# Performance work log

Hardware: AMD Instinct MI355X
Metric: run time of the kernel (lower is better)

Reference implementation:

```python
import jax, jax.numpy as jnp
import numpy as np

THRESH = 0.3   # vis_threshold (score filter and final keep threshold)
SIGMA = 0.5    # Gaussian soft-NMS sigma (method=2 in classic soft_nms)
B, N = 16, 2048


def setup_inputs() -> dict:
    key = jax.random.key(0)
    k1, k2, k3 = jax.random.split(key, 3)
    xy = jax.random.uniform(k1, (B, N, 2), dtype=jnp.float32) * 1024.0
    wh = jax.random.uniform(k2, (B, N, 2), dtype=jnp.float32) * 256.0 + 1.0
    scores = jax.random.uniform(k3, (B, N, 1), dtype=jnp.float32)
    detections = jnp.concatenate([xy, xy + wh, scores], axis=-1)  # [B,N,5]
    return {"detections": detections}


def _pairwise_iou(b):
    # b: [N,4] as (x1,y1,x2,y2); classic soft-NMS uses +1 area convention
    x1, y1, x2, y2 = b[:, 0], b[:, 1], b[:, 2], b[:, 3]
    area = (x2 - x1 + 1.0) * (y2 - y1 + 1.0)
    xx1 = jnp.maximum(x1[:, None], x1[None, :])
    yy1 = jnp.maximum(y1[:, None], y1[None, :])
    xx2 = jnp.minimum(x2[:, None], x2[None, :])
    yy2 = jnp.minimum(y2[:, None], y2[None, :])
    w = jnp.clip(xx2 - xx1 + 1.0, 0.0)
    h = jnp.clip(yy2 - yy1 + 1.0, 0.0)
    inter = w * h
    return inter / (area[:, None] + area[None, :] - inter)  # [N,N]


def _soft_nms_single(boxes, scores):
    # boxes: [N,4], scores: [N]
    n = scores.shape[0]
    iou = _pairwise_iou(boxes)            # [N,N]
    valid = scores > THRESH               # score-threshold prefilter
    s0 = jnp.where(valid, scores, 0.0)

    def step(carry, _):
        s, active = carry
        i = jnp.argmax(jnp.where(active, s, -1.0))     # greedy pick of max live score
        si = jnp.where(active[i], s[i], -1.0)          # -1 sentinel once all boxes consumed
        w = jnp.exp(-(iou[i] * iou[i]) / SIGMA)        # Gaussian decay (method=2)
        active = active.at[i].set(False)
        s = jnp.where(active, s * w, s)                # decay remaining live scores
        return (s, active), (i, si)

    _, (idx, picked) = jax.lax.scan(step, (s0, valid), None, length=n)
    # score each box carried at the moment it was picked; .max ignores -1 sentinels
    final = jnp.full((n,), -1.0, scores.dtype).at[idx].max(picked)
    keep = final > THRESH
    return final, keep


def reference(detections):
    boxes = detections[..., :4]   # [B,N,4]
    scores = detections[..., 4]   # [B,N]
    final, keep = jax.vmap(_soft_nms_single)(boxes, scores)
    return final, keep
```

## Files before the change

### kernel.cpp

```cpp
#include <hip/hip_runtime.h>
#include <stdint.h>

static constexpr float kThresh = 0.3f;
static constexpr float kFreeze = 0.0195f;
static constexpr int N    = 2048;
static constexpr int NT   = 256;
static constexpr int LPT  = N / NT;
static constexpr int NW   = NT / 64;
static constexpr int KMAX = 8;

using u64 = unsigned long long;
using u32 = unsigned int;

template <int CTRL>
__device__ __forceinline__ u64 dpp_max_u64_step(u64 k) {
    const int lo  = (int)(u32)k;
    const int hi  = (int)(u32)(k >> 32);
    const int mlo = __builtin_amdgcn_update_dpp(lo, lo, CTRL, 0xF, 0xF, false);
    const int mhi = __builtin_amdgcn_update_dpp(hi, hi, CTRL, 0xF, 0xF, false);
    const u64 m   = ((u64)(u32)mhi << 32) | (u32)mlo;
    return (m > k) ? m : k;
}
__device__ __forceinline__ u64 wave_max_u64(u64 k) {
    k = dpp_max_u64_step<0x111>(k);
    k = dpp_max_u64_step<0x112>(k);
    k = dpp_max_u64_step<0x114>(k);
    k = dpp_max_u64_step<0x118>(k);
    k = dpp_max_u64_step<0x142>(k);
    k = dpp_max_u64_step<0x143>(k);
    const int lo = __builtin_amdgcn_readlane((int)(u32)k, 63);
    const int hi = __builtin_amdgcn_readlane((int)(u32)(k >> 32), 63);
    return ((u64)(u32)hi << 32) | (u32)lo;
}

struct Pick {
    u32    mid;
    float4 box;
    float  area;
};

template <int K>
__device__ __forceinline__ u64 decay_and_keys(
        float (&sr)[KMAX], const float (&x1)[KMAX], const float (&y1)[KMAX],
        const float (&x2)[KMAX], const float (&y2)[KMAX], const float (&ar)[KMAX],
        const u32 (&jp)[KMAX], const Pick& w)
{
    u64 kmax = 0ULL;
    #pragma unroll
    for (int e = 0; e < K; ++e) {
        if (jp[e] == w.mid) sr[e] = -1.0f;
        const float xx1 = fmaxf(w.box.x, x1[e]);
        const float yy1 = fmaxf(w.box.y, y1[e]);
        const float xx2 = fminf(w.box.z, x2[e]);
        const float yy2 = fminf(w.box.w, y2[e]);
        const float ww  = fmaxf(xx2 - xx1 + 1.0f, 0.0f);
        const float hh  = fmaxf(yy2 - yy1 + 1.0f, 0.0f);
        const float inter = ww * hh;
        const float iou   = inter / (w.area + ar[e] - inter);
        sr[e] *= expf(-(iou * iou) * 2.0f);
        const u64 key = ((u64)(__float_as_uint(sr[e]) + 1u) << 32) | jp[e];
        const u64 kk  = (__float_as_int(sr[e]) >= 0) ? key : 0ULL;
        if (kk > kmax) kmax = kk;
    }
    return kmax;
}

template <int K>
__device__ __forceinline__ void fill_slots(
        float (&sr)[KMAX], float (&x1)[KMAX], float (&y1)[KMAX],
        float (&x2)[KMAX], float (&y2)[KMAX], float (&ar)[KMAX], u32 (&jp)[KMAX],
        const int* slist, const float* srs, const float4* sbox, int t, int alive)
{
    #pragma unroll
    for (int e = 0; e < K; ++e) {
        const int pos = t + NT * e;
        if (pos < alive) {
            const int j = slist[pos];
            sr[e] = srs[pos];
            const float4 bb = sbox[j];
            x1[e] = bb.x; y1[e] = bb.y; x2[e] = bb.z; y2[e] = bb.w;
            ar[e] = (bb.z - bb.x + 1.0f) * (bb.w - bb.y + 1.0f);
            jp[e] = ((u32)(N - 1 - j) << 21) | ((u32)t << 13) | ((u32)e << 10);
        } else {
            sr[e] = -1.0f;
            x1[e] = 3.0e38f; y1[e] = 3.0e38f; x2[e] = -3.0e38f; y2[e] = -3.0e38f;
            ar[e] = 1.0f;
            jp[e] = 0x3FFu;
        }
    }
}

template <int K>
__device__ __forceinline__ void run_tier(
        int& alive, int& k, Pick& w,
        float (&sr)[KMAX], float (&x1)[KMAX], float (&y1)[KMAX],
        float (&x2)[KMAX], float (&y2)[KMAX], float (&ar)[KMAX], u32 (&jp)[KMAX],
        int* slist, float* srs, const float4* sbox, float* sfin,
        u64 (*redk)[NW], int* swave, int t, int lane, int wid)
{
    const int floorA = (K > 1) ? NT * (K - 1) : 0;
    if (alive <= floorA) return;

    fill_slots<K>(sr, x1, y1, x2, y2, ar, jp, slist, srs, sbox, t, alive);
    const int tierFill = alive;

    while (alive > floorA) {
        const int par = k & 1;
        const u64 kmax = decay_and_keys<K>(sr, x1, y1, x2, y2, ar, jp, w);
        const u64 wmax = wave_max_u64(kmax);
        const bool writer = (wmax != 0ULL) ? (kmax == wmax) : (lane == 0);
        if (writer) redk[par][wid] = wmax;
        __syncthreads();
        u64 best = redk[par][0];
        #pragma unroll
        for (int q = 1; q < NW; ++q) {
            const u64 o = redk[par][q];
            if (o > best) best = o;
        }
        const u32   lo = (u32)best;
        const float v1 = __uint_as_float((u32)(best >> 32) - 1u);

        if (v1 < kFreeze) {
            #pragma unroll
            for (int e = 0; e < K; ++e) {
                const int pos = t + NT * e;
                if (pos < tierFill && __float_as_int(sr[e]) >= 0)
                    sfin[(N - 1) - (int)(jp[e] >> 21)] = sr[e];
            }
            alive = -1;
            return;
        }

        const int winJ = (N - 1) - (int)(lo >> 21);
        w.mid = lo;
        if (t == 0) sfin[winJ] = v1;
        w.box  = sbox[winJ];
        w.area = (w.box.z - w.box.x + 1.0f) * (w.box.w - w.box.y + 1.0f);
        --alive; ++k;
    }

    if (K > 1) {
        (void)decay_and_keys<K>(sr, x1, y1, x2, y2, ar, jp, w);
        w.mid  = 0xFFFFFFFFu;
        w.box  = make_float4(3.0e38f, 3.0e38f, -3.0e38f, -3.0e38f);
        w.area = 1.0f;
        int c = 0;
        #pragma unroll
        for (int e = 0; e < K; ++e) c += (__float_as_int(sr[e]) >= 0) ? 1 : 0;
        int pfx = c;
        #pragma unroll
        for (int d = 1; d < 64; d <<= 1) {
            const int v = __shfl_up(pfx, d, 64);
            if (lane >= d) pfx += v;
        }
        if (lane == 63) swave[wid] = pfx;
        __syncthreads();
        int wbase = 0;
        #pragma unroll
        for (int q = 0; q < NW; ++q)
            if (q < wid) wbase += swave[q];
        int mypos = wbase + (pfx - c);
        #pragma unroll
        for (int e = 0; e < K; ++e) {
            if (__float_as_int(sr[e]) >= 0) {
                slist[mypos] = (N - 1) - (int)(jp[e] >> 21);
                srs[mypos]   = sr[e];
                ++mypos;
            }
        }
        __syncthreads();
    }
}

__launch_bounds__(NT, 1)
__global__ void soft_nms_kernel(const float* __restrict__ det,
                                float* __restrict__ out, int B)
{
    const int b = blockIdx.x, t = threadIdx.x, lane = t & 63, wid = t >> 6;

    __shared__ float4 sbox[N];
    __shared__ float  sfin[N];
    __shared__ float  srs[N];
    __shared__ int    slist[N];
    __shared__ int    swave[NW];
    __shared__ u64    redk[2][NW];

    const float* dbase = det + (size_t)b * N * 5;

    float scv[LPT]; int lval = 0, c = 0;
    #pragma unroll
    for (int e = 0; e < LPT; ++e) {
        const int j = t * LPT + e;
        const float* p = dbase + (size_t)j * 5;
        const float X1 = p[0], Y1 = p[1], X2 = p[2], Y2 = p[3], SC = p[4];
        sbox[j]  = make_float4(X1, Y1, X2, Y2);
        sfin[j]  = -1.0f;
        scv[e]   = SC;
        const int va = SC > kThresh;
        lval |= va << e; c += va;
    }
    int pfx = c;
    #pragma unroll
    for (int d = 1; d < 64; d <<= 1) {
        const int v = __shfl_up(pfx, d, 64);
        if (lane >= d) pfx += v;
    }
    if (lane == 63) swave[wid] = pfx;
    __syncthreads();
    int wbase = 0, n0 = 0;
    #pragma unroll
    for (int q = 0; q < NW; ++q) {
        const int v = swave[q];
        if (q < wid) wbase += v;
        n0 += v;
    }
    int mypos = wbase + (pfx - c);
    #pragma unroll
    for (int e = 0; e < LPT; ++e)
        if ((lval >> e) & 1) { slist[mypos] = t * LPT + e; srs[mypos] = scv[e]; ++mypos; }
    __syncthreads();

    float sr[KMAX], x1[KMAX], y1[KMAX], x2[KMAX], y2[KMAX], ar[KMAX]; u32 jp[KMAX];
    int alive = n0, k = 0;
    Pick w;
    w.mid  = 0xFFFFFFFFu;
    w.box  = make_float4(3.0e38f, 3.0e38f, -3.0e38f, -3.0e38f);
    w.area = 1.0f;

    run_tier<8>(alive,k,w,sr,x1,y1,x2,y2,ar,jp,slist,srs,sbox,sfin,redk,swave,t,lane,wid);
    run_tier<7>(alive,k,w,sr,x1,y1,x2,y2,ar,jp,slist,srs,sbox,sfin,redk,swave,t,lane,wid);
    run_tier<6>(alive,k,w,sr,x1,y1,x2,y2,ar,jp,slist,srs,sbox,sfin,redk,swave,t,lane,wid);
    run_tier<5>(alive,k,w,sr,x1,y1,x2,y2,ar,jp,slist,srs,sbox,sfin,redk,swave,t,lane,wid);
    run_tier<4>(alive,k,w,sr,x1,y1,x2,y2,ar,jp,slist,srs,sbox,sfin,redk,swave,t,lane,wid);
    run_tier<3>(alive,k,w,sr,x1,y1,x2,y2,ar,jp,slist,srs,sbox,sfin,redk,swave,t,lane,wid);
    run_tier<2>(alive,k,w,sr,x1,y1,x2,y2,ar,jp,slist,srs,sbox,sfin,redk,swave,t,lane,wid);
    run_tier<1>(alive,k,w,sr,x1,y1,x2,y2,ar,jp,slist,srs,sbox,sfin,redk,swave,t,lane,wid);

    __syncthreads();
    float* of = out + (size_t)b * N;
    float* ok = out + (size_t)B * N + (size_t)b * N;
    #pragma unroll
    for (int e = 0; e < LPT; ++e) {
        const int j = t * LPT + e;
        const float f = sfin[j];
        of[j] = f;
        ok[j] = (f > kThresh) ? 1.0f : 0.0f;
    }
}

extern "C" void kernel_launch(void* const* d_in, const int* in_sizes, int n_in,
                              void* d_out, int out_size, void* d_ws, size_t ws_size,
                              hipStream_t stream) {
    const float* det = (const float*)d_in[0];
    float* out = (float*)d_out;
    const int B = in_sizes[0] / (N * 5);
    hipLaunchKernelGGL(soft_nms_kernel, dim3(B), dim3(NT), 0, stream, det, out, B);
}
```

Baseline: 930.4 us.

## Batch up to four mutually disjoint greedy picks per soft-NMS iteration

Each iteration now finds the top four live scores through per-thread top-4 insertion, four chained wave reductions and a merge across waves. It accepts the leading prefix of winners whose boxes do not overlap each other, since disjoint picks leave one another's scores unchanged. All accepted picks then decay the remaining scores in a single pass, so fewer serial iterations and block barriers are needed. The cost is four IoU/exp evaluations per element per iteration, plus extra reduction work and register pressure. It also assumes, without checking, that applying a disjoint pick's decay before the next one does not reorder the other scores.

```diff
diff --git a/kernel.cpp b/kernel.cpp
--- a/kernel.cpp
+++ b/kernel.cpp
@@ -3,11 +3,12 @@
 
 static constexpr float kThresh = 0.3f;
 static constexpr float kFreeze = 0.0195f;
-static constexpr int N    = 2048;
-static constexpr int NT   = 256;
-static constexpr int LPT  = N / NT;
-static constexpr int NW   = NT / 64;
-static constexpr int KMAX = 8;
+static constexpr int N     = 2048;
+static constexpr int NT    = 256;
+static constexpr int LPT   = N / NT;
+static constexpr int NW    = NT / 64;
+static constexpr int KMAX  = 8;
+static constexpr int NP    = 4;
 
 using u64 = unsigned long long;
 using u32 = unsigned int;
@@ -33,42 +34,59 @@
     return ((u64)(u32)hi << 32) | (u32)lo;
 }
 
-struct Pick {
-    u32    mid;
-    float4 box;
-    float  area;
+struct Picks {
+    int    mj[NP];
+    float4 box[NP];
+    float  area[NP];
 };
+__device__ __forceinline__ void picks_clear(Picks& P) {
+    #pragma unroll
+    for (int i = 0; i < NP; ++i) {
+        P.mj[i]   = -9;
+        P.box[i]  = make_float4(3.0e38f, 3.0e38f, -3.0e38f, -3.0e38f);
+        P.area[i] = 1.0f;
+    }
+}
 
 template <int K>
-__device__ __forceinline__ u64 decay_and_keys(
+__device__ __forceinline__ void decay_top4(
         float (&sr)[KMAX], const float (&x1)[KMAX], const float (&y1)[KMAX],
         const float (&x2)[KMAX], const float (&y2)[KMAX], const float (&ar)[KMAX],
-        const u32 (&jp)[KMAX], const Pick& w)
+        const int (&jr)[KMAX], const Picks& P, u64 (&a)[NP])
 {
-    u64 kmax = 0ULL;
+    a[0] = 0; a[1] = 0; a[2] = 0; a[3] = 0;
     #pragma unroll
     for (int e = 0; e < K; ++e) {
-        if (jp[e] == w.mid) sr[e] = -1.0f;
-        const float xx1 = fmaxf(w.box.x, x1[e]);
-        const float yy1 = fmaxf(w.box.y, y1[e]);
-        const float xx2 = fminf(w.box.z, x2[e]);
-        const float yy2 = fminf(w.box.w, y2[e]);
-        const float ww  = fmaxf(xx2 - xx1 + 1.0f, 0.0f);
-        const float hh  = fmaxf(yy2 - yy1 + 1.0f, 0.0f);
-        const float inter = ww * hh;
-        const float iou   = inter / (w.area + ar[e] - inter);
-        sr[e] *= expf(-(iou * iou) * 2.0f);
-        const u64 key = ((u64)(__float_as_uint(sr[e]) + 1u) << 32) | jp[e];
-        const u64 kk  = (__float_as_int(sr[e]) >= 0) ? key : 0ULL;
-        if (kk > kmax) kmax = kk;
-    }
-    return kmax;
+        const bool killed = (jr[e] == P.mj[0]) | (jr[e] == P.mj[1]) |
+                            (jr[e] == P.mj[2]) | (jr[e] == P.mj[3]);
+        if (killed) sr[e] = -1.0f;
+        #pragma unroll
+        for (int i = 0; i < NP; ++i) {
+            const float xx1 = fmaxf(P.box[i].x, x1[e]);
+            const float yy1 = fmaxf(P.box[i].y, y1[e]);
+            const float xx2 = fminf(P.box[i].z, x2[e]);
+            const float yy2 = fminf(P.box[i].w, y2[e]);
+            const float ww  = fmaxf(xx2 - xx1 + 1.0f, 0.0f);
+            const float hh  = fmaxf(yy2 - yy1 + 1.0f, 0.0f);
+            const float inter = ww * hh;
+            const float iou   = inter / (P.area[i] + ar[e] - inter);
+            sr[e] *= expf(-(iou * iou) * 2.0f);
+        }
+        const u64 key = ((u64)(__float_as_uint(sr[e]) + 1u) << 32)
+                      | (u32)(N - 1 - jr[e]);
+        const u64 kk = (__float_as_int(sr[e]) >= 0) ? key : 0ULL;
+        const bool g0 = kk > a[0], g1 = kk > a[1], g2 = kk > a[2], g3 = kk > a[3];
+        a[3] = g3 ? (g2 ? a[2] : kk) : a[3];
+        a[2] = g2 ? (g1 ? a[1] : kk) : a[2];
+        a[1] = g1 ? (g0 ? a[0] : kk) : a[1];
+        a[0] = g0 ? kk : a[0];
+    }
 }
 
 template <int K>
 __device__ __forceinline__ void fill_slots(
         float (&sr)[KMAX], float (&x1)[KMAX], float (&y1)[KMAX],
-        float (&x2)[KMAX], float (&y2)[KMAX], float (&ar)[KMAX], u32 (&jp)[KMAX],
+        float (&x2)[KMAX], float (&y2)[KMAX], float (&ar)[KMAX], int (&jr)[KMAX],
         const int* slist, const float* srs, const float4* sbox, int t, int alive)
 {
     #pragma unroll
@@ -80,74 +98,133 @@
             const float4 bb = sbox[j];
             x1[e] = bb.x; y1[e] = bb.y; x2[e] = bb.z; y2[e] = bb.w;
             ar[e] = (bb.z - bb.x + 1.0f) * (bb.w - bb.y + 1.0f);
-            jp[e] = ((u32)(N - 1 - j) << 21) | ((u32)t << 13) | ((u32)e << 10);
+            jr[e] = j;
         } else {
             sr[e] = -1.0f;
             x1[e] = 3.0e38f; y1[e] = 3.0e38f; x2[e] = -3.0e38f; y2[e] = -3.0e38f;
             ar[e] = 1.0f;
-            jp[e] = 0x3FFu;
+            jr[e] = -2;
         }
     }
 }
 
 template <int K>
 __device__ __forceinline__ void run_tier(
-        int& alive, int& k, Pick& w,
+        int& alive, int& k, Picks& P,
         float (&sr)[KMAX], float (&x1)[KMAX], float (&y1)[KMAX],
-        float (&x2)[KMAX], float (&y2)[KMAX], float (&ar)[KMAX], u32 (&jp)[KMAX],
-        int* slist, float* srs, const float4* sbox, float* sfin,
-        u64 (*redk)[NW], int* swave, int t, int lane, int wid)
+        float (&x2)[KMAX], float (&y2)[KMAX], float (&ar)[KMAX], int (&jr)[KMAX],
+        int* slist, float* srs, const float4* sbox, const float* sarea, float* sfin,
+        u64 (*redk)[NW][NP], int* swave, int t, int lane, int wid)
 {
     const int floorA = (K > 1) ? NT * (K - 1) : 0;
     if (alive <= floorA) return;
 
-    fill_slots<K>(sr, x1, y1, x2, y2, ar, jp, slist, srs, sbox, t, alive);
+    fill_slots<K>(sr, x1, y1, x2, y2, ar, jr, slist, srs, sbox, t, alive);
     const int tierFill = alive;
 
     while (alive > floorA) {
         const int par = k & 1;
-        const u64 kmax = decay_and_keys<K>(sr, x1, y1, x2, y2, ar, jp, w);
-        const u64 wmax = wave_max_u64(kmax);
-        const bool writer = (wmax != 0ULL) ? (kmax == wmax) : (lane == 0);
-        if (writer) redk[par][wid] = wmax;
+        u64 a[NP];
+        decay_top4<K>(sr, x1, y1, x2, y2, ar, jr, P, a);
+
+        u32 c = 0;
+        u64 wout[NP];
+        #pragma unroll
+        for (int r = 0; r < NP; ++r) {
+            const u64 cand = (c == 0u) ? a[0] : (c == 1u) ? a[1]
+                           : (c == 2u) ? a[2] : (c == 3u) ? a[3] : 0ULL;
+            const u64 m = wave_max_u64(cand);
+            wout[r] = m;
+            c += (m != 0ULL && cand == m) ? 1u : 0u;
+        }
+        if (lane == 0) {
+            redk[par][wid][0] = wout[0]; redk[par][wid][1] = wout[1];
+            redk[par][wid][2] = wout[2]; redk[par][wid][3] = wout[3];
+        }
         __syncthreads();
-        u64 best = redk[par][0];
-        #pragma unroll
-        for (int q = 1; q < NW; ++q) {
-            const u64 o = redk[par][q];
-            if (o > best) best = o;
-        }
-        const u32   lo = (u32)best;
-        const float v1 = __uint_as_float((u32)(best >> 32) - 1u);
+
+        u64 Ls[NW][NP];
+        #pragma unroll
+        for (int q = 0; q < NW; ++q)
+            #pragma unroll
+            for (int r = 0; r < NP; ++r) Ls[q][r] = redk[par][q][r];
+        int c0 = 0, c1 = 0, c2 = 0, c3 = 0;
+        u64 g[NP];
+        #pragma unroll
+        for (int r = 0; r < NP; ++r) {
+            const u64 d0 = (c0==0)?Ls[0][0]:(c0==1)?Ls[0][1]:(c0==2)?Ls[0][2]:(c0==3)?Ls[0][3]:0ULL;
+            const u64 d1 = (c1==0)?Ls[1][0]:(c1==1)?Ls[1][1]:(c1==2)?Ls[1][2]:(c1==3)?Ls[1][3]:0ULL;
+            const u64 d2 = (c2==0)?Ls[2][0]:(c2==1)?Ls[2][1]:(c2==2)?Ls[2][2]:(c2==3)?Ls[2][3]:0ULL;
+            const u64 d3 = (c3==0)?Ls[3][0]:(c3==1)?Ls[3][1]:(c3==2)?Ls[3][2]:(c3==3)?Ls[3][3]:0ULL;
+            u64 m = d0; int qs = 0;
+            if (d1 > m) { m = d1; qs = 1; }
+            if (d2 > m) { m = d2; qs = 2; }
+            if (d3 > m) { m = d3; qs = 3; }
+            g[r] = m;
+            c0 += (qs == 0); c1 += (qs == 1); c2 += (qs == 2); c3 += (qs == 3);
+        }
+        const float v1 = __uint_as_float((u32)(g[0] >> 32) - 1u);
 
         if (v1 < kFreeze) {
             #pragma unroll
             for (int e = 0; e < K; ++e) {
                 const int pos = t + NT * e;
                 if (pos < tierFill && __float_as_int(sr[e]) >= 0)
-                    sfin[(N - 1) - (int)(jp[e] >> 21)] = sr[e];
+                    sfin[jr[e]] = sr[e];
             }
             alive = -1;
             return;
         }
 
-        const int winJ = (N - 1) - (int)(lo >> 21);
-        w.mid = lo;
-        if (t == 0) sfin[winJ] = v1;
-        w.box  = sbox[winJ];
-        w.area = (w.box.z - w.box.x + 1.0f) * (w.box.w - w.box.y + 1.0f);
-        --alive; ++k;
+        int jg[NP]; float vg[NP]; bool nz[NP];
+        #pragma unroll
+        for (int r = 0; r < NP; ++r) {
+            nz[r] = (g[r] != 0ULL);
+            jg[r] = (N - 1) - (int)((u32)g[r] & 0x7FFu);
+            vg[r] = __uint_as_float((u32)(g[r] >> 32) - 1u);
+        }
+        float4 bb[NP]; float aa[NP];
+        #pragma unroll
+        for (int r = 0; r < NP; ++r) { bb[r] = sbox[jg[r]]; aa[r] = sarea[jg[r]]; }
+
+        #define DISJ(i, kx) \
+            ((fmaxf(fminf(bb[i].z, bb[kx].z) - fmaxf(bb[i].x, bb[kx].x) + 1.0f, 0.0f) * \
+              fmaxf(fminf(bb[i].w, bb[kx].w) - fmaxf(bb[i].y, bb[kx].y) + 1.0f, 0.0f)) == 0.0f)
+        int Lp = 1;
+        if (nz[1] && DISJ(0, 1)) {
+            Lp = 2;
+            if (nz[2] && DISJ(0, 2) && DISJ(1, 2)) {
+                Lp = 3;
+                if (nz[3] && DISJ(0, 3) && DISJ(1, 3) && DISJ(2, 3)) Lp = 4;
+            }
+        }
+        #undef DISJ
+
+        if (t == 0) {
+            sfin[jg[0]] = vg[0];
+            if (Lp > 1) sfin[jg[1]] = vg[1];
+            if (Lp > 2) sfin[jg[2]] = vg[2];
+            if (Lp > 3) sfin[jg[3]] = vg[3];
+        }
+        #pragma unroll
+        for (int r = 0; r < NP; ++r) {
+            const bool on = (r < Lp);
+            P.mj[r]   = on ? jg[r] : -9;
+            P.box[r]  = on ? bb[r] : make_float4(3.0e38f, 3.0e38f, -3.0e38f, -3.0e38f);
+            P.area[r] = on ? aa[r] : 1.0f;
+        }
+        alive -= Lp; ++k;
     }
 
     if (K > 1) {
-        (void)decay_and_keys<K>(sr, x1, y1, x2, y2, ar, jp, w);
-        w.mid  = 0xFFFFFFFFu;
-        w.box  = make_float4(3.0e38f, 3.0e38f, -3.0e38f, -3.0e38f);
-        w.area = 1.0f;
-        int c = 0;
-        #pragma unroll
-        for (int e = 0; e < K; ++e) c += (__float_as_int(sr[e]) >= 0) ? 1 : 0;
-        int pfx = c;
+        u64 atmp[NP];
+        decay_top4<K>(sr, x1, y1, x2, y2, ar, jr, P, atmp);
+        (void)atmp;
+        picks_clear(P);
+        int cc = 0;
+        #pragma unroll
+        for (int e = 0; e < K; ++e) cc += (__float_as_int(sr[e]) >= 0) ? 1 : 0;
+        int pfx = cc;
         #pragma unroll
         for (int d = 1; d < 64; d <<= 1) {
             const int v = __shfl_up(pfx, d, 64);
@@ -159,11 +236,11 @@
         #pragma unroll
         for (int q = 0; q < NW; ++q)
             if (q < wid) wbase += swave[q];
-        int mypos = wbase + (pfx - c);
+        int mypos = wbase + (pfx - cc);
         #pragma unroll
         for (int e = 0; e < K; ++e) {
             if (__float_as_int(sr[e]) >= 0) {
-                slist[mypos] = (N - 1) - (int)(jp[e] >> 21);
+                slist[mypos] = jr[e];
                 srs[mypos]   = sr[e];
                 ++mypos;
             }
@@ -179,11 +256,12 @@
     const int b = blockIdx.x, t = threadIdx.x, lane = t & 63, wid = t >> 6;
 
     __shared__ float4 sbox[N];
+    __shared__ float  sarea[N];
     __shared__ float  sfin[N];
     __shared__ float  srs[N];
     __shared__ int    slist[N];
     __shared__ int    swave[NW];
-    __shared__ u64    redk[2][NW];
+    __shared__ u64    redk[2][NW][NP];
 
     const float* dbase = det + (size_t)b * N * 5;
 
@@ -194,6 +272,7 @@
         const float* p = dbase + (size_t)j * 5;
         const float X1 = p[0], Y1 = p[1], X2 = p[2], Y2 = p[3], SC = p[4];
         sbox[j]  = make_float4(X1, Y1, X2, Y2);
+        sarea[j] = (X2 - X1 + 1.0f) * (Y2 - Y1 + 1.0f);
         sfin[j]  = -1.0f;
         scv[e]   = SC;
         const int va = SC > kThresh;
@@ -220,21 +299,19 @@
         if ((lval >> e) & 1) { slist[mypos] = t * LPT + e; srs[mypos] = scv[e]; ++mypos; }
     __syncthreads();
 
-    float sr[KMAX], x1[KMAX], y1[KMAX], x2[KMAX], y2[KMAX], ar[KMAX]; u32 jp[KMAX];
+    float sr[KMAX], x1[KMAX], y1[KMAX], x2[KMAX], y2[KMAX], ar[KMAX]; int jr[KMAX];
     int alive = n0, k = 0;
-    Pick w;
-    w.mid  = 0xFFFFFFFFu;
-    w.box  = make_float4(3.0e38f, 3.0e38f, -3.0e38f, -3.0e38f);
-    w.area = 1.0f;
-
-    run_tier<8>(alive,k,w,sr,x1,y1,x2,y2,ar,jp,slist,srs,sbox,sfin,redk,swave,t,lane,wid);
-    run_tier<7>(alive,k,w,sr,x1,y1,x2,y2,ar,jp,slist,srs,sbox,sfin,redk,swave,t,lane,wid);
-    run_tier<6>(alive,k,w,sr,x1,y1,x2,y2,ar,jp,slist,srs,sbox,sfin,redk,swave,t,lane,wid);
-    run_tier<5>(alive,k,w,sr,x1,y1,x2,y2,ar,jp,slist,srs,sbox,sfin,redk,swave,t,lane,wid);
-    run_tier<4>(alive,k,w,sr,x1,y1,x2,y2,ar,jp,slist,srs,sbox,sfin,redk,swave,t,lane,wid);
-    run_tier<3>(alive,k,w,sr,x1,y1,x2,y2,ar,jp,slist,srs,sbox,sfin,redk,swave,t,lane,wid);
-    run_tier<2>(alive,k,w,sr,x1,y1,x2,y2,ar,jp,slist,srs,sbox,sfin,redk,swave,t,lane,wid);
-    run_tier<1>(alive,k,w,sr,x1,y1,x2,y2,ar,jp,slist,srs,sbox,sfin,redk,swave,t,lane,wid);
+    Picks P;
+    picks_clear(P);
+
+    run_tier<8>(alive,k,P,sr,x1,y1,x2,y2,ar,jr,slist,srs,sbox,sarea,sfin,redk,swave,t,lane,wid);
+    run_tier<7>(alive,k,P,sr,x1,y1,x2,y2,ar,jr,slist,srs,sbox,sarea,sfin,redk,swave,t,lane,wid);
+    run_tier<6>(alive,k,P,sr,x1,y1,x2,y2,ar,jr,slist,srs,sbox,sarea,sfin,redk,swave,t,lane,wid);
+    run_tier<5>(alive,k,P,sr,x1,y1,x2,y2,ar,jr,slist,srs,sbox,sarea,sfin,redk,swave,t,lane,wid);
+    run_tier<4>(alive,k,P,sr,x1,y1,x2,y2,ar,jr,slist,srs,sbox,sarea,sfin,redk,swave,t,lane,wid);
+    run_tier<3>(alive,k,P,sr,x1,y1,x2,y2,ar,jr,slist,srs,sbox,sarea,sfin,redk,swave,t,lane,wid);
+    run_tier<2>(alive,k,P,sr,x1,y1,x2,y2,ar,jr,slist,srs,sbox,sarea,sfin,redk,swave,t,lane,wid);
+    run_tier<1>(alive,k,P,sr,x1,y1,x2,y2,ar,jr,slist,srs,sbox,sarea,sfin,redk,swave,t,lane,wid);
 
     __syncthreads();
     float* of = out + (size_t)b * N;
```

Measured after the change: 1.119 ms. 1.2x slower.
